# Optimization experiments

Hardware: AMD Instinct MI355X
Metric: run time of the kernel (lower is better)

## Reference

```python
import jax, jax.numpy as jnp
import numpy as np

NEG_INF = -1e30


def setup_inputs() -> dict:
    key = jax.random.key(0)
    kq, kk, kv, ks = jax.random.split(key, 4)
    B, H, S, D = 2, 16, 2048, 64
    return {
        "q": jax.random.normal(kq, (B, H, S, D), dtype=jnp.float32),
        "k": jax.random.normal(kk, (B, H, S, D), dtype=jnp.float32),
        "v": jax.random.normal(kv, (B, H, S, D), dtype=jnp.float32),
        "sink_weights": jax.random.normal(ks, (H,), dtype=jnp.float32),
        "sliding_window": 1024,
    }


def reference(q, k, v, sink_weights, sliding_window):
    """Sliding-window causal attention with a learnable attention-sink logit.

    Equivalent to FlexAttention.forward with sink_weights given: an extra kv
    position (the sink) is appended whose score is replaced by sink_weights[h]
    and whose value is zero -> it only adds mass to the softmax denominator.
    """
    B, H, S_q, D = q.shape
    S_kv = k.shape[2]
    scale = 1.0 / np.sqrt(D)

    # [B, H, S_q, S_kv] raw scores
    scores = jnp.einsum("bhqd,bhkd->bhqk", q, k) * scale

    q_idx = jnp.arange(S_q)[:, None]
    kv_idx = jnp.arange(S_kv)[None, :]
    keep = (kv_idx <= q_idx) & (q_idx - kv_idx <= sliding_window)  # [S_q, S_kv]
    scores = jnp.where(keep[None, None], scores, NEG_INF)

    # sink column: per-head learnable logit, always visible
    sink_col = jnp.broadcast_to(
        sink_weights[None, :, None, None], (B, H, S_q, 1)
    )
    logits = jnp.concatenate([scores, sink_col], axis=-1)  # [B,H,S_q,S_kv+1]

    probs = jax.nn.softmax(logits, axis=-1)
    # sink value is zero, so only the first S_kv prob columns hit v
    out = jnp.einsum("bhqk,bhkd->bhqd", probs[..., :S_kv], v)
    return out
```

## Files before the change

kernel.cpp:

```cpp
#include <hip/hip_runtime.h>


typedef __bf16 bf16x8 __attribute__((ext_vector_type(8)));
typedef __bf16 bf16x4 __attribute__((ext_vector_type(4)));
typedef float  f32x16 __attribute__((ext_vector_type(16)));

#define SK 72
#define SV 72
#define SPP 72
#define NT 128

__global__ __launch_bounds__(NT, 2) void flex_attn_mfma32(
    const float* __restrict__ Q, const float* __restrict__ K,
    const float* __restrict__ V, const float* __restrict__ SINKW,
    const int* __restrict__ SWIN, float* __restrict__ OUT,
    const int H, const int S)
{
    const int t    = threadIdx.x;
    const int lane = t & 63;
    const int g    = t >> 6;
    const int c    = lane & 31;
    const int hl   = lane >> 5;
    const int qt   = blockIdx.x;
    const int bh   = blockIdx.y;
    const int h    = bh % H;
    const int q0   = qt * 64;
    const int qw0  = q0 + 32 * g;
    const int W    = SWIN[0];
    const float scale = 0.125f;

    __shared__ __align__(16) __bf16 k_lds[64 * SK];
    __shared__ __align__(16) __bf16 v_lds[64 * SV];
    __shared__ __align__(16) __bf16 p_lds[2 * 32 * SPP];

    const size_t basebh = (size_t)bh * S * 64;

    bf16x8 bq[4];
    {
        const float4* qp4 = (const float4*)(Q + basebh + (size_t)(qw0 + c) * 64);
        #pragma unroll
        for (int ks = 0; ks < 4; ++ks) {
            float4 f0 = qp4[4 * ks + 2 * hl];
            float4 f1 = qp4[4 * ks + 2 * hl + 1];
            bq[ks][0] = (__bf16)(f0.x * scale); bq[ks][1] = (__bf16)(f0.y * scale);
            bq[ks][2] = (__bf16)(f0.z * scale); bq[ks][3] = (__bf16)(f0.w * scale);
            bq[ks][4] = (__bf16)(f1.x * scale); bq[ks][5] = (__bf16)(f1.y * scale);
            bq[ks][6] = (__bf16)(f1.z * scale); bq[ks][7] = (__bf16)(f1.w * scale);
        }
    }

    const int dg = t & 15;
    const int kg = t >> 4;
    const float4* kp4 = (const float4*)(K + basebh);
    const float4* vp4 = (const float4*)(V + basebh);
    float4 kreg[8], vreg[8];

    auto load_tiles = [&](int kt) {
        #pragma unroll
        for (int i = 0; i < 8; ++i)
            kreg[i] = kp4[kt * 1024 + i * NT + t];
        #pragma unroll
        for (int r = 0; r < 2; ++r)
            #pragma unroll
            for (int kk = 0; kk < 4; ++kk)
                vreg[4 * r + kk] = vp4[kt * 1024 + (32 * r + 4 * kg + kk) * 16 + dg];
    };

    auto stage_tiles = [&]() {
        #pragma unroll
        for (int i = 0; i < 8; ++i) {
            const int flat = i * NT + t;
            const int key = flat >> 4, dd = flat & 15;
            float4 f = kreg[i];
            bf16x4 b = { (__bf16)f.x, (__bf16)f.y, (__bf16)f.z, (__bf16)f.w };
            *(bf16x4*)&k_lds[key * SK + 4 * dd] = b;
        }
        #pragma unroll
        for (int r = 0; r < 2; ++r) {
            float4 a0 = vreg[4*r+0], a1 = vreg[4*r+1], a2 = vreg[4*r+2], a3 = vreg[4*r+3];
            const int kb = 32 * r + 4 * kg;
            bf16x4 w0 = { (__bf16)a0.x, (__bf16)a1.x, (__bf16)a2.x, (__bf16)a3.x };
            bf16x4 w1 = { (__bf16)a0.y, (__bf16)a1.y, (__bf16)a2.y, (__bf16)a3.y };
            bf16x4 w2 = { (__bf16)a0.z, (__bf16)a1.z, (__bf16)a2.z, (__bf16)a3.z };
            bf16x4 w3 = { (__bf16)a0.w, (__bf16)a1.w, (__bf16)a2.w, (__bf16)a3.w };
            *(bf16x4*)&v_lds[(4 * dg + 0) * SV + kb] = w0;
            *(bf16x4*)&v_lds[(4 * dg + 1) * SV + kb] = w1;
            *(bf16x4*)&v_lds[(4 * dg + 2) * SV + kb] = w2;
            *(bf16x4*)&v_lds[(4 * dg + 3) * SV + kb] = w3;
        }
    };

    float mrun = SINKW[h];
    float lrun = 1.0f;
    f32x16 accO0, accO1;
    #pragma unroll
    for (int i = 0; i < 16; ++i) { accO0[i] = 0.0f; accO1[i] = 0.0f; }

    int lo = q0 - W; if (lo < 0) lo = 0;
    const int kt0 = lo >> 6, kt1 = qt;

    load_tiles(kt0);

    for (int kt = kt0; kt <= kt1; ++kt) {
        __syncthreads();
        stage_tiles();
        if (kt < kt1) load_tiles(kt + 1);
        __syncthreads();

        const int k0 = kt * 64;

        f32x16 accS0, accS1;
        #pragma unroll
        for (int i = 0; i < 16; ++i) { accS0[i] = 0.0f; accS1[i] = 0.0f; }
        #pragma unroll
        for (int ks = 0; ks < 4; ++ks) {
            bf16x8 ka0 = *(const bf16x8*)&k_lds[c * SK + 16 * ks + 8 * hl];
            bf16x8 ka1 = *(const bf16x8*)&k_lds[(32 + c) * SK + 16 * ks + 8 * hl];
            accS0 = __builtin_amdgcn_mfma_f32_32x32x16_bf16(ka0, bq[ks], accS0, 0, 0, 0);
            accS1 = __builtin_amdgcn_mfma_f32_32x32x16_bf16(ka1, bq[ks], accS1, 0, 0, 0);
        }

        const bool interior = (k0 + 63 <= qw0) && (qw0 + 31 - k0 <= W);
        if (!interior) {
            const int qi = qw0 + c;
            #pragma unroll
            for (int rg = 0; rg < 16; ++rg) {
                const int kb  = (rg & 3) + 8 * (rg >> 2) + 4 * hl;
                const int ki0 = k0 + kb, ki1 = k0 + 32 + kb;
                if (!((ki0 <= qi) && (qi - ki0 <= W))) accS0[rg] = -1e30f;
                if (!((ki1 <= qi) && (qi - ki1 <= W))) accS1[rg] = -1e30f;
            }
        }

        float mx = accS0[0];
        #pragma unroll
        for (int i = 1; i < 16; ++i) mx = fmaxf(mx, accS0[i]);
        #pragma unroll
        for (int i = 0; i < 16; ++i) mx = fmaxf(mx, accS1[i]);
        mx = fmaxf(mx, __shfl_xor(mx, 32, 64));
        const float mnew  = fmaxf(mrun, mx);
        const float alpha = __expf(mrun - mnew);
        float ps = 0.0f;
        #pragma unroll
        for (int i = 0; i < 16; ++i) { float p = __expf(accS0[i] - mnew); accS0[i] = p; ps += p; }
        #pragma unroll
        for (int i = 0; i < 16; ++i) { float p = __expf(accS1[i] - mnew); accS1[i] = p; ps += p; }
        ps += __shfl_xor(ps, 32, 64);
        lrun = lrun * alpha + ps;
        mrun = mnew;
        #pragma unroll
        for (int i = 0; i < 16; ++i) { accO0[i] *= alpha; accO1[i] *= alpha; }

        __bf16* pw = p_lds + g * 32 * SPP;
        #pragma unroll
        for (int rg = 0; rg < 4; ++rg) {
            bf16x4 b0 = { (__bf16)accS0[4*rg+0], (__bf16)accS0[4*rg+1],
                          (__bf16)accS0[4*rg+2], (__bf16)accS0[4*rg+3] };
            bf16x4 b1 = { (__bf16)accS1[4*rg+0], (__bf16)accS1[4*rg+1],
                          (__bf16)accS1[4*rg+2], (__bf16)accS1[4*rg+3] };
            *(bf16x4*)&pw[c * SPP +      8 * rg + 4 * hl] = b0;
            *(bf16x4*)&pw[c * SPP + 32 + 8 * rg + 4 * hl] = b1;
        }

        #pragma unroll
        for (int ks = 0; ks < 4; ++ks) {
            bf16x8 bp  = *(const bf16x8*)&pw[c * SPP + 16 * ks + 8 * hl];
            bf16x8 va0 = *(const bf16x8*)&v_lds[c * SV + 16 * ks + 8 * hl];
            bf16x8 va1 = *(const bf16x8*)&v_lds[(32 + c) * SV + 16 * ks + 8 * hl];
            accO0 = __builtin_amdgcn_mfma_f32_32x32x16_bf16(va0, bp, accO0, 0, 0, 0);
            accO1 = __builtin_amdgcn_mfma_f32_32x32x16_bf16(va1, bp, accO1, 0, 0, 0);
        }
    }

    const float inv = 1.0f / lrun;
    float* ob = OUT + basebh + (size_t)(qw0 + c) * 64;
    #pragma unroll
    for (int rg = 0; rg < 4; ++rg) {
        float4 f0 = { accO0[4*rg+0]*inv, accO0[4*rg+1]*inv, accO0[4*rg+2]*inv, accO0[4*rg+3]*inv };
        float4 f1 = { accO1[4*rg+0]*inv, accO1[4*rg+1]*inv, accO1[4*rg+2]*inv, accO1[4*rg+3]*inv };
        *(float4*)&ob[     8 * rg + 4 * hl] = f0;
        *(float4*)&ob[32 + 8 * rg + 4 * hl] = f1;
    }
}

extern "C" void kernel_launch(void* const* d_in, const int* in_sizes, int n_in,
                              void* d_out, int out_size, void* d_ws, size_t ws_size,
                              hipStream_t stream) {
    const float* q     = (const float*)d_in[0];
    const float* k     = (const float*)d_in[1];
    const float* v     = (const float*)d_in[2];
    const float* sinkw = (const float*)d_in[3];
    const int*   swin  = (const int*)d_in[4];
    float* out = (float*)d_out;

    const int H = in_sizes[3];
    const int S = 2048;
    const int B = in_sizes[0] / (H * S * 64);

    dim3 grid(S / 64, B * H);
    flex_attn_mfma32<<<grid, NT, 0, stream>>>(q, k, v, sinkw, swin, out, H, S);
}
```

Before: 147.7 us.

## Rewrite attention with 16x16 MFMA, 4-wave blocks and paired-tile load balancing

```diff
diff --git a/kernel.cpp b/kernel.cpp
--- a/kernel.cpp
+++ b/kernel.cpp
@@ -3,183 +3,200 @@
 
 typedef __bf16 bf16x8 __attribute__((ext_vector_type(8)));
 typedef __bf16 bf16x4 __attribute__((ext_vector_type(4)));
-typedef float  f32x16 __attribute__((ext_vector_type(16)));
+typedef float  f32x4  __attribute__((ext_vector_type(4)));
 
 #define SK 72
 #define SV 72
 #define SPP 72
-#define NT 128
-
-__global__ __launch_bounds__(NT, 2) void flex_attn_mfma32(
+#define SO 68
+#define NT 256
+
+__global__ __launch_bounds__(NT, 3) void flex_attn_r4(
     const float* __restrict__ Q, const float* __restrict__ K,
     const float* __restrict__ V, const float* __restrict__ SINKW,
     const int* __restrict__ SWIN, float* __restrict__ OUT,
-    const int H, const int S)
+    const int H, const int S, const int NBH)
 {
     const int t    = threadIdx.x;
     const int lane = t & 63;
-    const int g    = t >> 6;
-    const int c    = lane & 31;
-    const int hl   = lane >> 5;
-    const int qt   = blockIdx.x;
-    const int bh   = blockIdx.y;
-    const int h    = bh % H;
-    const int q0   = qt * 64;
-    const int qw0  = q0 + 32 * g;
+    const int w    = t >> 6;
+    const int r    = lane & 15;
+    const int quad = lane >> 4;
     const int W    = SWIN[0];
     const float scale = 0.125f;
 
-    __shared__ __align__(16) __bf16 k_lds[64 * SK];
-    __shared__ __align__(16) __bf16 v_lds[64 * SV];
-    __shared__ __align__(16) __bf16 p_lds[2 * 32 * SPP];
+    __shared__ __align__(16) unsigned char smem[27648];
+    __bf16* k_lds = (__bf16*)smem;
+    __bf16* v_lds = (__bf16*)(smem + 9216);
+    __bf16* p_lds = (__bf16*)(smem + 18432);
+    float*  o_lds = (float*)smem;
+
+    const int id = blockIdx.x;
+    int bh, qtA, qtB, nphase;
+    if (id < NBH * 16) {
+        bh = id >> 4; qtA = 16 + (id & 15); qtB = 0; nphase = 1;
+    } else {
+        const int j = id - NBH * 16;
+        bh = j >> 3; const int p = j & 7;
+        qtA = p; qtB = 15 - p; nphase = 2;
+    }
 
     const size_t basebh = (size_t)bh * S * 64;
-
-    bf16x8 bq[4];
-    {
-        const float4* qp4 = (const float4*)(Q + basebh + (size_t)(qw0 + c) * 64);
-        #pragma unroll
-        for (int ks = 0; ks < 4; ++ks) {
-            float4 f0 = qp4[4 * ks + 2 * hl];
-            float4 f1 = qp4[4 * ks + 2 * hl + 1];
-            bq[ks][0] = (__bf16)(f0.x * scale); bq[ks][1] = (__bf16)(f0.y * scale);
-            bq[ks][2] = (__bf16)(f0.z * scale); bq[ks][3] = (__bf16)(f0.w * scale);
-            bq[ks][4] = (__bf16)(f1.x * scale); bq[ks][5] = (__bf16)(f1.y * scale);
-            bq[ks][6] = (__bf16)(f1.z * scale); bq[ks][7] = (__bf16)(f1.w * scale);
-        }
-    }
-
-    const int dg = t & 15;
-    const int kg = t >> 4;
+    const int h = bh % H;
+    const float sw = SINKW[h];
     const float4* kp4 = (const float4*)(K + basebh);
     const float4* vp4 = (const float4*)(V + basebh);
-    float4 kreg[8], vreg[8];
-
-    auto load_tiles = [&](int kt) {
-        #pragma unroll
-        for (int i = 0; i < 8; ++i)
-            kreg[i] = kp4[kt * 1024 + i * NT + t];
-        #pragma unroll
-        for (int r = 0; r < 2; ++r)
-            #pragma unroll
-            for (int kk = 0; kk < 4; ++kk)
-                vreg[4 * r + kk] = vp4[kt * 1024 + (32 * r + 4 * kg + kk) * 16 + dg];
-    };
-
-    auto stage_tiles = [&]() {
-        #pragma unroll
-        for (int i = 0; i < 8; ++i) {
-            const int flat = i * NT + t;
-            const int key = flat >> 4, dd = flat & 15;
-            float4 f = kreg[i];
-            bf16x4 b = { (__bf16)f.x, (__bf16)f.y, (__bf16)f.z, (__bf16)f.w };
-            *(bf16x4*)&k_lds[key * SK + 4 * dd] = b;
+    const int dgi = t & 15;
+    const int kgi = t >> 4;
+
+    float4 kreg[4], vreg[4];
+
+    for (int ph = 0; ph < nphase; ++ph) {
+        const int qt  = ph ? qtB : qtA;
+        const int q0  = qt * 64;
+        const int qw0 = q0 + 16 * w;
+        const int qi  = qw0 + r;
+
+        bf16x8 bq[2];
+        {
+            const float4* qp4 = (const float4*)(Q + basebh + (size_t)qi * 64);
+            #pragma unroll
+            for (int ks = 0; ks < 2; ++ks) {
+                float4 f0 = qp4[8 * ks + 2 * quad];
+                float4 f1 = qp4[8 * ks + 2 * quad + 1];
+                bq[ks][0] = (__bf16)(f0.x * scale); bq[ks][1] = (__bf16)(f0.y * scale);
+                bq[ks][2] = (__bf16)(f0.z * scale); bq[ks][3] = (__bf16)(f0.w * scale);
+                bq[ks][4] = (__bf16)(f1.x * scale); bq[ks][5] = (__bf16)(f1.y * scale);
+                bq[ks][6] = (__bf16)(f1.z * scale); bq[ks][7] = (__bf16)(f1.w * scale);
+            }
         }
-        #pragma unroll
-        for (int r = 0; r < 2; ++r) {
-            float4 a0 = vreg[4*r+0], a1 = vreg[4*r+1], a2 = vreg[4*r+2], a3 = vreg[4*r+3];
-            const int kb = 32 * r + 4 * kg;
-            bf16x4 w0 = { (__bf16)a0.x, (__bf16)a1.x, (__bf16)a2.x, (__bf16)a3.x };
-            bf16x4 w1 = { (__bf16)a0.y, (__bf16)a1.y, (__bf16)a2.y, (__bf16)a3.y };
-            bf16x4 w2 = { (__bf16)a0.z, (__bf16)a1.z, (__bf16)a2.z, (__bf16)a3.z };
-            bf16x4 w3 = { (__bf16)a0.w, (__bf16)a1.w, (__bf16)a2.w, (__bf16)a3.w };
-            *(bf16x4*)&v_lds[(4 * dg + 0) * SV + kb] = w0;
-            *(bf16x4*)&v_lds[(4 * dg + 1) * SV + kb] = w1;
-            *(bf16x4*)&v_lds[(4 * dg + 2) * SV + kb] = w2;
-            *(bf16x4*)&v_lds[(4 * dg + 3) * SV + kb] = w3;
+
+        float mrun = sw, lrun = 1.0f;
+        f32x4 accO[4];
+        #pragma unroll
+        for (int i = 0; i < 4; ++i) { accO[i].x = 0.f; accO[i].y = 0.f; accO[i].z = 0.f; accO[i].w = 0.f; }
+
+        int lo = q0 - W; if (lo < 0) lo = 0;
+        const int kt0 = lo >> 6, kt1 = qt;
+
+        #pragma unroll
+        for (int i = 0; i < 4; ++i) kreg[i] = kp4[kt0 * 1024 + i * NT + t];
+        #pragma unroll
+        for (int kk = 0; kk < 4; ++kk) vreg[kk] = vp4[kt0 * 1024 + (4 * kgi + kk) * 16 + dgi];
+
+        for (int kt = kt0; kt <= kt1; ++kt) {
+            const int k0 = kt * 64;
+            __syncthreads();
+
+            #pragma unroll
+            for (int i = 0; i < 4; ++i) {
+                const int flat = i * NT + t;
+                const int key = flat >> 4, dd = flat & 15;
+                float4 f = kreg[i];
+                bf16x4 b = { (__bf16)f.x, (__bf16)f.y, (__bf16)f.z, (__bf16)f.w };
+                *(bf16x4*)&k_lds[key * SK + 4 * dd] = b;
+            }
+            {
+                float4 a0 = vreg[0], a1 = vreg[1], a2 = vreg[2], a3 = vreg[3];
+                bf16x4 w0 = { (__bf16)a0.x, (__bf16)a1.x, (__bf16)a2.x, (__bf16)a3.x };
+                bf16x4 w1 = { (__bf16)a0.y, (__bf16)a1.y, (__bf16)a2.y, (__bf16)a3.y };
+                bf16x4 w2 = { (__bf16)a0.z, (__bf16)a1.z, (__bf16)a2.z, (__bf16)a3.z };
+                bf16x4 w3 = { (__bf16)a0.w, (__bf16)a1.w, (__bf16)a2.w, (__bf16)a3.w };
+                *(bf16x4*)&v_lds[(4 * dgi + 0) * SV + 4 * kgi] = w0;
+                *(bf16x4*)&v_lds[(4 * dgi + 1) * SV + 4 * kgi] = w1;
+                *(bf16x4*)&v_lds[(4 * dgi + 2) * SV + 4 * kgi] = w2;
+                *(bf16x4*)&v_lds[(4 * dgi + 3) * SV + 4 * kgi] = w3;
+            }
+            if (kt < kt1) {
+                #pragma unroll
+                for (int i = 0; i < 4; ++i) kreg[i] = kp4[(kt + 1) * 1024 + i * NT + t];
+                #pragma unroll
+                for (int kk = 0; kk < 4; ++kk) vreg[kk] = vp4[(kt + 1) * 1024 + (4 * kgi + kk) * 16 + dgi];
+            }
+            __syncthreads();
+
+            f32x4 accS[4];
+            #pragma unroll
+            for (int n = 0; n < 4; ++n) { accS[n].x = 0.f; accS[n].y = 0.f; accS[n].z = 0.f; accS[n].w = 0.f; }
+            #pragma unroll
+            for (int ks = 0; ks < 2; ++ks)
+                #pragma unroll
+                for (int n = 0; n < 4; ++n) {
+                    bf16x8 ka = *(const bf16x8*)&k_lds[(n * 16 + r) * SK + ks * 32 + quad * 8];
+                    accS[n] = __builtin_amdgcn_mfma_f32_16x16x32_bf16(ka, bq[ks], accS[n], 0, 0, 0);
+                }
+
+            const bool interior = (k0 + 63 <= qw0) && (qw0 + 15 - k0 <= W);
+            if (!interior) {
+                #pragma unroll
+                for (int n = 0; n < 4; ++n)
+                    #pragma unroll
+                    for (int reg = 0; reg < 4; ++reg) {
+                        const int key = k0 + n * 16 + 4 * quad + reg;
+                        if (!((key <= qi) && (qi - key <= W))) accS[n][reg] = -1e30f;
+                    }
+            }
+
+            float mx = fmaxf(fmaxf(accS[0][0], accS[0][1]), fmaxf(accS[0][2], accS[0][3]));
+            #pragma unroll
+            for (int n = 1; n < 4; ++n)
+                mx = fmaxf(mx, fmaxf(fmaxf(accS[n][0], accS[n][1]), fmaxf(accS[n][2], accS[n][3])));
+            mx = fmaxf(mx, __shfl_xor(mx, 16, 64));
+            mx = fmaxf(mx, __shfl_xor(mx, 32, 64));
+            const float mnew  = fmaxf(mrun, mx);
+            const float alpha = __expf(mrun - mnew);
+            float ps = 0.0f;
+            #pragma unroll
+            for (int n = 0; n < 4; ++n)
+                #pragma unroll
+                for (int reg = 0; reg < 4; ++reg) {
+                    const float p = __expf(accS[n][reg] - mnew);
+                    accS[n][reg] = p;
+                    ps += p;
+                }
+            ps += __shfl_xor(ps, 16, 64);
+            ps += __shfl_xor(ps, 32, 64);
+            lrun = lrun * alpha + ps;
+            mrun = mnew;
+            #pragma unroll
+            for (int n = 0; n < 4; ++n) {
+                accO[n].x *= alpha; accO[n].y *= alpha; accO[n].z *= alpha; accO[n].w *= alpha;
+            }
+
+            __bf16* pw = p_lds + w * 16 * SPP;
+            #pragma unroll
+            for (int n = 0; n < 4; ++n) {
+                bf16x4 b = { (__bf16)accS[n][0], (__bf16)accS[n][1],
+                             (__bf16)accS[n][2], (__bf16)accS[n][3] };
+                *(bf16x4*)&pw[r * SPP + n * 16 + 4 * quad] = b;
+            }
+
+            #pragma unroll
+            for (int ks = 0; ks < 2; ++ks) {
+                bf16x8 bp = *(const bf16x8*)&pw[r * SPP + ks * 32 + quad * 8];
+                #pragma unroll
+                for (int dt = 0; dt < 4; ++dt) {
+                    bf16x8 va = *(const bf16x8*)&v_lds[(dt * 16 + r) * SV + ks * 32 + quad * 8];
+                    accO[dt] = __builtin_amdgcn_mfma_f32_16x16x32_bf16(va, bp, accO[dt], 0, 0, 0);
+                }
+            }
         }
-    };
-
-    float mrun = SINKW[h];
-    float lrun = 1.0f;
-    f32x16 accO0, accO1;
-    #pragma unroll
-    for (int i = 0; i < 16; ++i) { accO0[i] = 0.0f; accO1[i] = 0.0f; }
-
-    int lo = q0 - W; if (lo < 0) lo = 0;
-    const int kt0 = lo >> 6, kt1 = qt;
-
-    load_tiles(kt0);
-
-    for (int kt = kt0; kt <= kt1; ++kt) {
+
         __syncthreads();
-        stage_tiles();
-        if (kt < kt1) load_tiles(kt + 1);
-        __syncthreads();
-
-        const int k0 = kt * 64;
-
-        f32x16 accS0, accS1;
-        #pragma unroll
-        for (int i = 0; i < 16; ++i) { accS0[i] = 0.0f; accS1[i] = 0.0f; }
-        #pragma unroll
-        for (int ks = 0; ks < 4; ++ks) {
-            bf16x8 ka0 = *(const bf16x8*)&k_lds[c * SK + 16 * ks + 8 * hl];
-            bf16x8 ka1 = *(const bf16x8*)&k_lds[(32 + c) * SK + 16 * ks + 8 * hl];
-            accS0 = __builtin_amdgcn_mfma_f32_32x32x16_bf16(ka0, bq[ks], accS0, 0, 0, 0);
-            accS1 = __builtin_amdgcn_mfma_f32_32x32x16_bf16(ka1, bq[ks], accS1, 0, 0, 0);
+        float* ow = o_lds + w * 16 * SO;
+        const float inv = 1.0f / lrun;
+        #pragma unroll
+        for (int dt = 0; dt < 4; ++dt)
+            #pragma unroll
+            for (int reg = 0; reg < 4; ++reg)
+                ow[r * SO + dt * 16 + 4 * quad + reg] = accO[dt][reg] * inv;
+        const int q2 = lane >> 2, j4 = lane & 3;
+        float* dst = OUT + basebh + (size_t)(qw0 + q2) * 64;
+        #pragma unroll
+        for (int c2 = 0; c2 < 4; ++c2) {
+            float4 vv = *(const float4*)&ow[q2 * SO + c2 * 16 + j4 * 4];
+            *(float4*)&dst[c2 * 16 + j4 * 4] = vv;
         }
-
-        const bool interior = (k0 + 63 <= qw0) && (qw0 + 31 - k0 <= W);
-        if (!interior) {
-            const int qi = qw0 + c;
-            #pragma unroll
-            for (int rg = 0; rg < 16; ++rg) {
-                const int kb  = (rg & 3) + 8 * (rg >> 2) + 4 * hl;
-                const int ki0 = k0 + kb, ki1 = k0 + 32 + kb;
-                if (!((ki0 <= qi) && (qi - ki0 <= W))) accS0[rg] = -1e30f;
-                if (!((ki1 <= qi) && (qi - ki1 <= W))) accS1[rg] = -1e30f;
-            }
-        }
-
-        float mx = accS0[0];
-        #pragma unroll
-        for (int i = 1; i < 16; ++i) mx = fmaxf(mx, accS0[i]);
-        #pragma unroll
-        for (int i = 0; i < 16; ++i) mx = fmaxf(mx, accS1[i]);
-        mx = fmaxf(mx, __shfl_xor(mx, 32, 64));
-        const float mnew  = fmaxf(mrun, mx);
-        const float alpha = __expf(mrun - mnew);
-        float ps = 0.0f;
-        #pragma unroll
-        for (int i = 0; i < 16; ++i) { float p = __expf(accS0[i] - mnew); accS0[i] = p; ps += p; }
-        #pragma unroll
-        for (int i = 0; i < 16; ++i) { float p = __expf(accS1[i] - mnew); accS1[i] = p; ps += p; }
-        ps += __shfl_xor(ps, 32, 64);
-        lrun = lrun * alpha + ps;
-        mrun = mnew;
-        #pragma unroll
-        for (int i = 0; i < 16; ++i) { accO0[i] *= alpha; accO1[i] *= alpha; }
-
-        __bf16* pw = p_lds + g * 32 * SPP;
-        #pragma unroll
-        for (int rg = 0; rg < 4; ++rg) {
-            bf16x4 b0 = { (__bf16)accS0[4*rg+0], (__bf16)accS0[4*rg+1],
-                          (__bf16)accS0[4*rg+2], (__bf16)accS0[4*rg+3] };
-            bf16x4 b1 = { (__bf16)accS1[4*rg+0], (__bf16)accS1[4*rg+1],
-                          (__bf16)accS1[4*rg+2], (__bf16)accS1[4*rg+3] };
-            *(bf16x4*)&pw[c * SPP +      8 * rg + 4 * hl] = b0;
-            *(bf16x4*)&pw[c * SPP + 32 + 8 * rg + 4 * hl] = b1;
-        }
-
-        #pragma unroll
-        for (int ks = 0; ks < 4; ++ks) {
-            bf16x8 bp  = *(const bf16x8*)&pw[c * SPP + 16 * ks + 8 * hl];
-            bf16x8 va0 = *(const bf16x8*)&v_lds[c * SV + 16 * ks + 8 * hl];
-            bf16x8 va1 = *(const bf16x8*)&v_lds[(32 + c) * SV + 16 * ks + 8 * hl];
-            accO0 = __builtin_amdgcn_mfma_f32_32x32x16_bf16(va0, bp, accO0, 0, 0, 0);
-            accO1 = __builtin_amdgcn_mfma_f32_32x32x16_bf16(va1, bp, accO1, 0, 0, 0);
-        }
-    }
-
-    const float inv = 1.0f / lrun;
-    float* ob = OUT + basebh + (size_t)(qw0 + c) * 64;
-    #pragma unroll
-    for (int rg = 0; rg < 4; ++rg) {
-        float4 f0 = { accO0[4*rg+0]*inv, accO0[4*rg+1]*inv, accO0[4*rg+2]*inv, accO0[4*rg+3]*inv };
-        float4 f1 = { accO1[4*rg+0]*inv, accO1[4*rg+1]*inv, accO1[4*rg+2]*inv, accO1[4*rg+3]*inv };
-        *(float4*)&ob[     8 * rg + 4 * hl] = f0;
-        *(float4*)&ob[32 + 8 * rg + 4 * hl] = f1;
     }
 }
 
@@ -196,7 +213,8 @@
     const int H = in_sizes[3];
     const int S = 2048;
     const int B = in_sizes[0] / (H * S * 64);
-
-    dim3 grid(S / 64, B * H);
-    flex_attn_mfma32<<<grid, NT, 0, stream>>>(q, k, v, sinkw, swin, out, H, S);
+    const int NBH = B * H;
+
+    dim3 grid(NBH * 24);
+    flex_attn_r4<<<grid, NT, 0, stream>>>(q, k, v, sinkw, swin, out, H, S, NBH);
 }
```

Measured after the change: 153.3 us. 1.04x slower.
